# Optimization experiments

Measured on AMD Instinct MI355X. Metric: run time of the kernel, lower is better.

The kernel has to match this reference:

```python
import jax, jax.numpy as jnp
import numpy as np

B, S, H, P2 = 64, 512, 768, 46  # batch, seq, hidden, num_p*2


def setup_inputs() -> dict:
    key = jax.random.key(0)
    k1, k2, k3, k4 = jax.random.split(key, 4)
    hidden_states = jax.random.normal(k1, (B, S, H), dtype=jnp.float32)
    # subject start/end indices must lie within the valid (masked-in) prefix
    lengths = jax.random.randint(k2, (B,), S // 4, S + 1)  # cue lengths per sample
    input_mask = (jnp.arange(S)[None, :] < lengths[:, None]).astype(jnp.int32)
    ids = jax.random.randint(k3, (B, 2), 0, S // 4)
    batch_subject_ids = jnp.sort(ids, axis=1).astype(jnp.int32)
    W = jax.random.normal(k4, (P2, H), dtype=jnp.float32) * (1.0 / np.sqrt(H))
    b = jnp.zeros((P2,), dtype=jnp.float32)
    return {"hidden_states": hidden_states, "batch_subject_ids": batch_subject_ids,
            "input_mask": input_mask, "W": W, "b": b}


def reference(hidden_states, batch_subject_ids, input_mask, W, b):
    # per-sample subject embedding: h[b, start] + h[b, end]  -> [B, H]
    batch_idx = jnp.arange(hidden_states.shape[0])
    s = (hidden_states[batch_idx, batch_subject_ids[:, 0]]
         + hidden_states[batch_idx, batch_subject_ids[:, 1]])
    # broadcast-add s to the first cue_len positions of each sample
    cue_len = jnp.sum(input_mask, axis=1)  # [B]
    pos_mask = (jnp.arange(hidden_states.shape[1])[None, :] < cue_len[:, None])  # [B, S]
    h = hidden_states + s[:, None, :] * pos_mask[:, :, None].astype(hidden_states.dtype)
    # linear + sigmoid^4 (dropout is identity in eval mode)
    logits = jnp.einsum('bsh,ph->bsp', h, W) + b
    return jax.nn.sigmoid(logits) ** 4
```

## Files before the change

kernel.cpp:

```cpp
#include <hip/hip_runtime.h>

#define SEQ 512
#define HID 768
#define P2  46
#define MT  64
#define BLK 256
#define NSTEP (HID / 32)
#define WROWS 48

typedef short bf16x8 __attribute__((ext_vector_type(8)));
typedef float f32x4  __attribute__((ext_vector_type(4)));

__device__ __forceinline__ unsigned short f2bf(float f) {
  union { float f; unsigned int u; } v; v.f = f;
  return (unsigned short)((v.u + 0x7FFFu + ((v.u >> 16) & 1u)) >> 16);
}

__global__ __launch_bounds__(BLK, 2) void fused_kernel(
    const float* __restrict__ h, const int* __restrict__ ids,
    const int* __restrict__ mask, const float* __restrict__ W,
    const float* __restrict__ bias, float* __restrict__ out) {

  __shared__ __align__(16) unsigned short wB[WROWS][HID];
  __shared__ float q_s[P2];

  const int tid  = threadIdx.x;
  const int lane = tid & 63, wv = tid >> 6;
  const int mr = lane & 15, qd = lane >> 4;
  const int row0 = blockIdx.x * MT;
  const int b    = row0 >> 9;

  #pragma unroll
  for (int i = 0; i < 35; ++i) {
    int idx = tid + i * BLK;
    if (idx < P2 * 192) {
      int p  = idx / 192;
      int c4 = idx - p * 192;
      float4 v = *(const float4*)(W + (size_t)p * HID + (c4 << 2));
      ushort4 u;
      u.x = f2bf(v.x); u.y = f2bf(v.y); u.z = f2bf(v.z); u.w = f2bf(v.w);
      int c  = c4 >> 1;
      int cs = (c & 0x78) | ((c ^ p) & 7);
      *(ushort4*)&wB[p][(cs << 3) + ((c4 & 1) << 2)] = u;
    }
  }

  {
    const int i0 = ids[b * 2 + 0], i1 = ids[b * 2 + 1];
    const float* r0p = h + ((size_t)b * SEQ + i0) * HID;
    const float* r1p = h + ((size_t)b * SEQ + i1) * HID;
    for (int p = wv; p < P2; p += 4) {
      const float* wp = W + (size_t)p * HID;
      float a = 0.f;
      #pragma unroll
      for (int j = 0; j < HID / 64; ++j) {
        int k = lane + (j << 6);
        a += (r0p[k] + r1p[k]) * wp[k];
      }
      #pragma unroll
      for (int off = 32; off > 0; off >>= 1) a += __shfl_xor(a, off, 64);
      if (lane == 0) q_s[p] = a;
    }
  }

  const int arow = row0 + (wv << 4) + mr;
  const float* abase = h + (size_t)arow * HID + (qd << 3);
  float4 pa[4][2];
  #pragma unroll
  for (int s = 0; s < 4; ++s) {
    pa[s][0] = *(const float4*)(abase + (s << 5));
    pa[s][1] = *(const float4*)(abase + (s << 5) + 4);
  }

  __syncthreads();

  f32x4 acc[3];
  #pragma unroll
  for (int nt = 0; nt < 3; ++nt) acc[nt] = f32x4{0.f, 0.f, 0.f, 0.f};

  #pragma unroll
  for (int s = 0; s < NSTEP; ++s) {
    float4 c0 = pa[s & 3][0], c1 = pa[s & 3][1];
    if (s + 4 < NSTEP) {
      pa[s & 3][0] = *(const float4*)(abase + ((s + 4) << 5));
      pa[s & 3][1] = *(const float4*)(abase + ((s + 4) << 5) + 4);
    }
    bf16x8 a = { (short)f2bf(c0.x), (short)f2bf(c0.y),
                 (short)f2bf(c0.z), (short)f2bf(c0.w),
                 (short)f2bf(c1.x), (short)f2bf(c1.y),
                 (short)f2bf(c1.z), (short)f2bf(c1.w) };
    int c  = (s << 2) + qd;
    int cs = (c & 0x78) | ((c ^ mr) & 7);
    #pragma unroll
    for (int nt = 0; nt < 3; ++nt) {
      bf16x8 bb = *(const bf16x8*)&wB[(nt << 4) + mr][cs << 3];
      acc[nt] = __builtin_amdgcn_mfma_f32_16x16x32_bf16(a, bb, acc[nt], 0, 0, 0);
    }
  }

  const int rbase = row0 + (wv << 4) + (qd << 2);
  int msk[4];
  #pragma unroll
  for (int i = 0; i < 4; ++i) msk[i] = mask[rbase + i];

  #pragma unroll
  for (int nt = 0; nt < 3; ++nt) {
    int p = (nt << 4) + mr;
    if (p < P2) {
      float bv = bias[p], qv = q_s[p];
      #pragma unroll
      for (int i = 0; i < 4; ++i) {
        float x = acc[nt][i] + bv + (msk[i] ? qv : 0.f);
        float sg = 1.f / (1.f + __expf(-x));
        sg *= sg; sg *= sg;
        out[(size_t)(rbase + i) * P2 + p] = sg;
      }
    }
  }
}

extern "C" void kernel_launch(void* const* d_in, const int* in_sizes, int n_in,
                              void* d_out, int out_size, void* d_ws, size_t ws_size,
                              hipStream_t stream) {
  const float* h    = (const float*)d_in[0];
  const int*   ids  = (const int*)d_in[1];
  const int*   mask = (const int*)d_in[2];
  const float* W    = (const float*)d_in[3];
  const float* bias = (const float*)d_in[4];
  float* out = (float*)d_out;

  fused_kernel<<<dim3((64 * SEQ) / MT), BLK, 0, stream>>>(h, ids, mask, W, bias, out);
}
```

Baseline: 166.6 us.

## Split W conversion and subject projection into prep kernel; stream W fragments from global

Adds a small prep kernel that converts W to bf16 once and computes the per-batch subject projection q, both written to workspace. The main GEMM kernel no longer has every block redo the W conversion, the LDS staging and the q dot products. It now reads W fragments straight from global/L2 with a two-step prefetch and an eight-step prefetch for h. MFMA operands are swapped so each lane holds consecutive output columns, which allows float2 stores. The cost is an extra kernel launch, a workspace round-trip, and W reads from L2 instead of LDS; padding rows 46–47 of the workspace are never written.

```diff
diff --git a/kernel.cpp b/kernel.cpp
--- a/kernel.cpp
+++ b/kernel.cpp
@@ -1,4 +1,5 @@
 #include <hip/hip_runtime.h>
+#include <hip/hip_bf16.h>
 
 #define SEQ 512
 #define HID 768
@@ -6,7 +7,7 @@
 #define MT  64
 #define BLK 256
 #define NSTEP (HID / 32)
-#define WROWS 48
+#define QSTRIDE 48
 
 typedef short bf16x8 __attribute__((ext_vector_type(8)));
 typedef float f32x4  __attribute__((ext_vector_type(4)));
@@ -16,63 +17,62 @@
   return (unsigned short)((v.u + 0x7FFFu + ((v.u >> 16) & 1u)) >> 16);
 }
 
-__global__ __launch_bounds__(BLK, 2) void fused_kernel(
+__device__ __forceinline__ short fcvt(float f) {
+  __hip_bfloat16 x = __float2bfloat16(f);
+  return *reinterpret_cast<short*>(&x);
+}
+
+__global__ __launch_bounds__(64) void prep_kernel(
     const float* __restrict__ h, const int* __restrict__ ids,
-    const int* __restrict__ mask, const float* __restrict__ W,
-    const float* __restrict__ bias, float* __restrict__ out) {
+    const float* __restrict__ W, unsigned short* __restrict__ Wb,
+    float* __restrict__ q) {
+  int b = blockIdx.x, p = blockIdx.y, lane = threadIdx.x;
+  const float* w = W + (size_t)p * HID;
+  if (b == 0) {
+    #pragma unroll
+    for (int j = 0; j < HID / 64; ++j)
+      Wb[p * HID + lane + j * 64] = f2bf(w[lane + j * 64]);
+  }
+  int i0 = ids[b * 2 + 0], i1 = ids[b * 2 + 1];
+  const float* r0 = h + ((size_t)b * SEQ + i0) * HID;
+  const float* r1 = h + ((size_t)b * SEQ + i1) * HID;
+  float acc = 0.f;
+  #pragma unroll
+  for (int j = 0; j < HID / 64; ++j) {
+    int k = lane + j * 64;
+    acc += (r0[k] + r1[k]) * w[k];
+  }
+  #pragma unroll
+  for (int off = 32; off > 0; off >>= 1) acc += __shfl_down(acc, off, 64);
+  if (lane == 0) q[b * QSTRIDE + p] = acc;
+}
 
-  __shared__ __align__(16) unsigned short wB[WROWS][HID];
-  __shared__ float q_s[P2];
-
+__global__ __launch_bounds__(BLK, 2) void main_kernel(
+    const float* __restrict__ h, const int* __restrict__ mask,
+    const unsigned short* __restrict__ Wb, const float* __restrict__ bias,
+    const float* __restrict__ q, float* __restrict__ out) {
   const int tid  = threadIdx.x;
   const int lane = tid & 63, wv = tid >> 6;
   const int mr = lane & 15, qd = lane >> 4;
   const int row0 = blockIdx.x * MT;
   const int b    = row0 >> 9;
+  const int row  = row0 + (wv << 4) + mr;
 
+  const float* hb = h + (size_t)row * HID + (qd << 3);
+  const unsigned short* wb = Wb + mr * HID + (qd << 3);
+
+  float4 ph[8][2];
   #pragma unroll
-  for (int i = 0; i < 35; ++i) {
-    int idx = tid + i * BLK;
-    if (idx < P2 * 192) {
-      int p  = idx / 192;
-      int c4 = idx - p * 192;
-      float4 v = *(const float4*)(W + (size_t)p * HID + (c4 << 2));
-      ushort4 u;
-      u.x = f2bf(v.x); u.y = f2bf(v.y); u.z = f2bf(v.z); u.w = f2bf(v.w);
-      int c  = c4 >> 1;
-      int cs = (c & 0x78) | ((c ^ p) & 7);
-      *(ushort4*)&wB[p][(cs << 3) + ((c4 & 1) << 2)] = u;
-    }
+  for (int s = 0; s < 8; ++s) {
+    ph[s][0] = *(const float4*)(hb + (s << 5));
+    ph[s][1] = *(const float4*)(hb + (s << 5) + 4);
   }
-
-  {
-    const int i0 = ids[b * 2 + 0], i1 = ids[b * 2 + 1];
-    const float* r0p = h + ((size_t)b * SEQ + i0) * HID;
-    const float* r1p = h + ((size_t)b * SEQ + i1) * HID;
-    for (int p = wv; p < P2; p += 4) {
-      const float* wp = W + (size_t)p * HID;
-      float a = 0.f;
-      #pragma unroll
-      for (int j = 0; j < HID / 64; ++j) {
-        int k = lane + (j << 6);
-        a += (r0p[k] + r1p[k]) * wp[k];
-      }
-      #pragma unroll
-      for (int off = 32; off > 0; off >>= 1) a += __shfl_xor(a, off, 64);
-      if (lane == 0) q_s[p] = a;
-    }
-  }
-
-  const int arow = row0 + (wv << 4) + mr;
-  const float* abase = h + (size_t)arow * HID + (qd << 3);
-  float4 pa[4][2];
+  bf16x8 pw[2][3];
   #pragma unroll
-  for (int s = 0; s < 4; ++s) {
-    pa[s][0] = *(const float4*)(abase + (s << 5));
-    pa[s][1] = *(const float4*)(abase + (s << 5) + 4);
-  }
-
-  __syncthreads();
+  for (int s = 0; s < 2; ++s)
+    #pragma unroll
+    for (int nt = 0; nt < 3; ++nt)
+      pw[s][nt] = *(const bf16x8*)(wb + nt * 16 * HID + (s << 5));
 
   f32x4 acc[3];
   #pragma unroll
@@ -80,42 +80,42 @@
 
   #pragma unroll
   for (int s = 0; s < NSTEP; ++s) {
-    float4 c0 = pa[s & 3][0], c1 = pa[s & 3][1];
-    if (s + 4 < NSTEP) {
-      pa[s & 3][0] = *(const float4*)(abase + ((s + 4) << 5));
-      pa[s & 3][1] = *(const float4*)(abase + ((s + 4) << 5) + 4);
+    float4 c0 = ph[s & 7][0], c1 = ph[s & 7][1];
+    if (s + 8 < NSTEP) {
+      ph[s & 7][0] = *(const float4*)(hb + ((s + 8) << 5));
+      ph[s & 7][1] = *(const float4*)(hb + ((s + 8) << 5) + 4);
     }
-    bf16x8 a = { (short)f2bf(c0.x), (short)f2bf(c0.y),
-                 (short)f2bf(c0.z), (short)f2bf(c0.w),
-                 (short)f2bf(c1.x), (short)f2bf(c1.y),
-                 (short)f2bf(c1.z), (short)f2bf(c1.w) };
-    int c  = (s << 2) + qd;
-    int cs = (c & 0x78) | ((c ^ mr) & 7);
-    #pragma unroll
-    for (int nt = 0; nt < 3; ++nt) {
-      bf16x8 bb = *(const bf16x8*)&wB[(nt << 4) + mr][cs << 3];
-      acc[nt] = __builtin_amdgcn_mfma_f32_16x16x32_bf16(a, bb, acc[nt], 0, 0, 0);
+    bf16x8 hfrag = { fcvt(c0.x), fcvt(c0.y), fcvt(c0.z), fcvt(c0.w),
+                     fcvt(c1.x), fcvt(c1.y), fcvt(c1.z), fcvt(c1.w) };
+    bf16x8 w0 = pw[s & 1][0], w1 = pw[s & 1][1], w2 = pw[s & 1][2];
+    if (s + 2 < NSTEP) {
+      #pragma unroll
+      for (int nt = 0; nt < 3; ++nt)
+        pw[s & 1][nt] = *(const bf16x8*)(wb + nt * 16 * HID + ((s + 2) << 5));
     }
+    acc[0] = __builtin_amdgcn_mfma_f32_16x16x32_bf16(w0, hfrag, acc[0], 0, 0, 0);
+    acc[1] = __builtin_amdgcn_mfma_f32_16x16x32_bf16(w1, hfrag, acc[1], 0, 0, 0);
+    acc[2] = __builtin_amdgcn_mfma_f32_16x16x32_bf16(w2, hfrag, acc[2], 0, 0, 0);
   }
 
-  const int rbase = row0 + (wv << 4) + (qd << 2);
-  int msk[4];
-  #pragma unroll
-  for (int i = 0; i < 4; ++i) msk[i] = mask[rbase + i];
-
+  const int mk = mask[row];
+  float* orow = out + (size_t)row * P2;
+  const float* qrow = q + b * QSTRIDE;
   #pragma unroll
   for (int nt = 0; nt < 3; ++nt) {
-    int p = (nt << 4) + mr;
-    if (p < P2) {
-      float bv = bias[p], qv = q_s[p];
-      #pragma unroll
-      for (int i = 0; i < 4; ++i) {
-        float x = acc[nt][i] + bv + (msk[i] ? qv : 0.f);
-        float sg = 1.f / (1.f + __expf(-x));
-        sg *= sg; sg *= sg;
-        out[(size_t)(rbase + i) * P2 + p] = sg;
-      }
+    const int p0 = (nt << 4) + (qd << 2);
+    float o[4];
+    #pragma unroll
+    for (int i = 0; i < 4; ++i) {
+      float bv = (p0 + i < P2) ? bias[p0 + i] : 0.f;
+      float qv = qrow[p0 + i];
+      float x = acc[nt][i] + bv + (mk ? qv : 0.f);
+      float sg = 1.f / (1.f + __expf(-x));
+      sg *= sg; sg *= sg;
+      o[i] = sg;
     }
+    if (p0 + 1 < P2) *(float2*)(orow + p0)     = make_float2(o[0], o[1]);
+    if (p0 + 3 < P2) *(float2*)(orow + p0 + 2) = make_float2(o[2], o[3]);
   }
 }
 
@@ -129,5 +129,9 @@
   const float* bias = (const float*)d_in[4];
   float* out = (float*)d_out;
 
-  fused_kernel<<<dim3((64 * SEQ) / MT), BLK, 0, stream>>>(h, ids, mask, W, bias, out);
+  unsigned short* Wb = (unsigned short*)d_ws;
+  float* q = (float*)((char*)d_ws + 48 * HID * sizeof(unsigned short));
+
+  prep_kernel<<<dim3(64, P2), 64, 0, stream>>>(h, ids, W, Wb, q);
+  main_kernel<<<dim3((64 * SEQ) / MT), BLK, 0, stream>>>(h, mask, Wb, bias, q, out);
 }
```

Result: no change. 166.1 us (-0.3%).
